# Kernel optimization log

Hardware: AMD Instinct MI355X
Metric: run time of the kernel (lower is better)

## Reference

```python
import jax, jax.numpy as jnp
import numpy as np

N = 10000   # num_nodes
E = 640000  # num_edges (avg degree 64)
IN = 128    # in_feature
HID = 16    # hidden (fixed in __init__)
H = 8       # out_head
ED = 8      # edge_dim
OUT = 3     # out_feature
SLOPE = 0.2 # LeakyReLU alpha in NGATConv

def setup_inputs():
    key = jax.random.key(0)
    k = jax.random.split(key, 16)
    def rn(i, shape, scale=1.0):
        return jax.random.normal(k[i], shape, dtype=jnp.float32) * jnp.float32(scale)
    return {
        "x": rn(0, (N, IN)),
        "edge_attr": rn(1, (E, ED)),
        "fc_w": rn(2, (HID, IN), 1.0 / np.sqrt(IN)),
        "fc_b": jnp.zeros((HID,), jnp.float32),
        "lin_w": rn(3, (H * HID, HID), 1.0 / np.sqrt(HID)),
        "att_src": rn(4, (H, HID), 0.1),
        "att_dst": rn(5, (H, HID), 0.1),
        "att_edge": rn(6, (H, HID), 0.1),
        "lin_edge_w": rn(7, (H * HID, ED), 1.0 / np.sqrt(ED)),
        "conv_bias": jnp.zeros((HID,), jnp.float32),
        "attn_fc_w": rn(8, (1, HID), 1.0 / np.sqrt(HID)),
        "attn_fc_b": jnp.zeros((1,), jnp.float32),
        "out_w": rn(9, (OUT, N * HID), 1.0 / np.sqrt(N * HID)),
        "out_b": jnp.zeros((OUT,), jnp.float32),
        "edge_index": jax.random.randint(k[10], (2, E), 0, N),
    }

def reference(x, edge_attr, fc_w, fc_b, lin_w, att_src, att_dst, att_edge,
              lin_edge_w, conv_bias, attn_fc_w, attn_fc_b, out_w, out_b, edge_index):
    src, dst = edge_index[0], edge_index[1]
    # embed (matrix_in=False path); dropout is identity in eval mode
    h = x @ fc_w.T + fc_b                                   # [N, HID]
    # NGATConv: per-head linear transform
    xp = (h @ lin_w.T).reshape(N, H, HID)                   # [N, H, C]
    a_src = jnp.einsum('nhc,hc->nh', xp, att_src)           # [N, H]
    a_dst = jnp.einsum('nhc,hc->nh', xp, att_dst)           # [N, H]
    ee = (edge_attr @ lin_edge_w.T).reshape(E, H, HID)      # [E, H, C]
    a_edge = jnp.einsum('ehc,hc->eh', ee, att_edge)         # [E, H]
    logits = a_src[src] + a_dst[dst] + a_edge               # [E, H]
    logits = jnp.where(logits >= 0, logits, SLOPE * logits) # LeakyReLU(0.2)
    # segment softmax over incoming edges of each destination node
    m = jax.ops.segment_max(logits, dst, num_segments=N)    # [N, H]
    ex = jnp.exp(logits - m[dst])
    denom = jax.ops.segment_sum(ex, dst, num_segments=N)    # [N, H]
    alpha = ex / (denom[dst] + 1e-16)                       # [E, H]
    # message passing: gather source features, weight, scatter-add to dst
    msg = alpha[:, :, None] * xp[src]                       # [E, H, C]
    agg = jax.ops.segment_sum(msg, dst, num_segments=N)     # [N, H, C]
    out = agg.mean(axis=1) + conv_bias                      # concat=False -> head mean
    out = jax.nn.elu(out)                                   # [N, HID]
    # attention pooling over nodes
    score = out @ attn_fc_w.T + attn_fc_b                   # [N, 1]
    w = jax.nn.softmax(score, axis=0)[:, 0]                 # softmax over node dim
    flat = (out * w[:, None]).reshape(1, -1)                # [1, N*HID]
    y = (flat @ out_w.T + out_b)[0]                         # [OUT]
    # attention weight element [head 0, dst 6, src 6]
    attn_66 = jnp.sum(jnp.where((src == 6) & (dst == 6), alpha[:, 0], jnp.float32(0.0)))
    return y, attn_66
```

## Files before the change

kernel.cpp:

```cpp
#include <hip/hip_runtime.h>
#include <hip/hip_fp16.h>

#define IN_F 128
#define HIDC 16
#define NHEAD 8
#define HHID 128
#define EDIM 8
#define MAXN 10240
#define HB   64
#define FB   128

__global__ __launch_bounds__(256) void k_node_hist(const float* __restrict__ x,
                                                   const float* __restrict__ fc_w,
                                                   const float* __restrict__ fc_b,
                                                   const float* __restrict__ lin_w,
                                                   const float* __restrict__ att_src,
                                                   const float* __restrict__ att_dst,
                                                   const int* __restrict__ ei,
                                                   __half* __restrict__ xp_h,
                                                   float* __restrict__ a_src,
                                                   float* __restrict__ a_dst,
                                                   unsigned short* __restrict__ ph,
                                                   unsigned short* __restrict__ lrank,
                                                   int N, int E, int CHUNK) {
    __shared__ __align__(16) char smem[MAXN * 4];
    int t = threadIdx.x;

    if ((int)blockIdx.x < HB) {
        int* lh = (int*)smem;
        int b = blockIdx.x;
        for (int i = t; i < MAXN; i += 256) lh[i] = 0;
        __syncthreads();
        int e0 = b * CHUNK;
        int e1 = min(e0 + CHUNK, E);
        for (int e = e0 + t; e < e1; e += 256)
            lrank[e] = (unsigned short)atomicAdd(&lh[ei[E + e]], 1);
        __syncthreads();
        for (int nn = t; nn < N; nn += 256)
            ph[(size_t)b * N + nn] = (unsigned short)lh[nn];
        return;
    }

    float* s_x   = (float*)smem;
    float* s_fc  = s_x + 32 * 129;
    float* s_lin = s_fc + 16 * 129;
    float* s_h   = s_lin + 128 * 17;
    float* s_as  = s_h + 32 * 17;
    float* s_ad  = s_as + HHID;
    float* s_fcb = s_ad + HHID;

    int n0 = (blockIdx.x - HB) * 32;

    for (int i = t; i < HIDC * IN_F; i += 256) s_fc[(i >> 7) * 129 + (i & 127)] = fc_w[i];
    for (int i = t; i < HHID * HIDC; i += 256) s_lin[(i >> 4) * 17 + (i & 15)] = lin_w[i];
    if (t < HHID) { s_as[t] = att_src[t]; s_ad[t] = att_dst[t]; }
    if (t < HIDC) s_fcb[t] = fc_b[t];
    for (int i = t; i < 32 * IN_F; i += 256) {
        size_t g = (size_t)n0 * IN_F + i;
        s_x[(i >> 7) * 129 + (i & 127)] = (g < (size_t)N * IN_F) ? x[g] : 0.f;
    }
    __syncthreads();

    {
        int k = t >> 5, n_l = t & 31;
        float a0 = 0.f, a1 = 0.f;
        #pragma unroll 8
        for (int d = 0; d < IN_F; ++d) {
            float xv = s_x[n_l * 129 + d];
            a0 += xv * s_fc[k * 129 + d];
            a1 += xv * s_fc[(k + 8) * 129 + d];
        }
        s_h[n_l * 17 + k]     = a0 + s_fcb[k];
        s_h[n_l * 17 + k + 8] = a1 + s_fcb[k + 8];
    }
    __syncthreads();

    int head = t >> 5, n_l = t & 31;
    int n = n0 + n_l;
    if (n >= N) return;

    float hreg[HIDC];
    #pragma unroll
    for (int k = 0; k < HIDC; ++k) hreg[k] = s_h[n_l * 17 + k];

    float as = 0.f, ad = 0.f;
    unsigned int pk[8];
    #pragma unroll
    for (int c2 = 0; c2 < 8; ++c2) {
        float v2[2];
        #pragma unroll
        for (int u = 0; u < 2; ++u) {
            int c = c2 * 2 + u;
            int j = head * HIDC + c;
            float v = 0.f;
            #pragma unroll
            for (int k = 0; k < HIDC; ++k) v += hreg[k] * s_lin[j * 17 + k];
            v2[u] = v;
            as += v * s_as[j];
            ad += v * s_ad[j];
        }
        unsigned short lo = __half_as_ushort(__float2half_rn(v2[0]));
        unsigned short hi = __half_as_ushort(__float2half_rn(v2[1]));
        pk[c2] = (unsigned int)lo | ((unsigned int)hi << 16);
    }
    __half* xph = xp_h + (size_t)n * HHID + head * HIDC;
    *(uint4*)(xph)     = make_uint4(pk[0], pk[1], pk[2], pk[3]);
    *(uint4*)(xph + 8) = make_uint4(pk[4], pk[5], pk[6], pk[7]);
    a_src[n * NHEAD + head] = as;
    a_dst[n * NHEAD + head] = ad;
}

__global__ __launch_bounds__(256) void k_coloff0(unsigned short* __restrict__ ph,
                                                 int* __restrict__ deg, int N) {
    int n = blockIdx.x * 256 + threadIdx.x;
    if (n >= N) return;
    unsigned short v[HB];
    #pragma unroll
    for (int b = 0; b < HB; ++b) v[b] = ph[(size_t)b * N + n];
    int run = 0;
    #pragma unroll
    for (int b = 0; b < HB; ++b) {
        int c = v[b];
        ph[(size_t)b * N + n] = (unsigned short)run;
        run += c;
    }
    deg[n] = run;
}

__global__ __launch_bounds__(1024) void k_scan(const int* __restrict__ deg,
                                               int* __restrict__ start, int N) {
    const int CH = 16;
    __shared__ int s_w[16];
    int t = threadIdx.x;
    int lane = t & 63, wid = t >> 6;
    int vals[CH];
    int base_i = t * CH;
    int s = 0;
    #pragma unroll
    for (int i = 0; i < CH; ++i) {
        int idx = base_i + i;
        int v = (idx < N) ? deg[idx] : 0;
        vals[i] = v;
        s += v;
    }
    int inc = s;
    #pragma unroll
    for (int off = 1; off < 64; off <<= 1) {
        int u = __shfl_up(inc, off, 64);
        if (lane >= off) inc += u;
    }
    if (lane == 63) s_w[wid] = inc;
    __syncthreads();
    if (wid == 0) {
        int wv = (lane < 16) ? s_w[lane] : 0;
        #pragma unroll
        for (int off = 1; off < 16; off <<= 1) {
            int u = __shfl_up(wv, off, 64);
            if (lane >= off) wv += u;
        }
        if (lane < 16) s_w[lane] = wv;
    }
    __syncthreads();
    int base = inc - s + (wid > 0 ? s_w[wid - 1] : 0);
    #pragma unroll
    for (int i = 0; i < CH; ++i) {
        int idx = base_i + i;
        if (idx < N) start[idx] = base;
        base += vals[i];
    }
    if (t == 0) start[N] = s_w[15];
}

__global__ __launch_bounds__(256) void k_fill(const float* __restrict__ ea,
                                              const int* __restrict__ ei,
                                              const float* __restrict__ a_src,
                                              const float* __restrict__ a_dst,
                                              const float* __restrict__ att_edge,
                                              const float* __restrict__ lin_edge_w,
                                              const int* __restrict__ start,
                                              const unsigned short* __restrict__ ph,
                                              const unsigned short* __restrict__ lrank,
                                              uint4* __restrict__ rec,
                                              int N, int E, int CHUNK) {
    __shared__ float s_w[64];
    int t = threadIdx.x;
    if (t < 64) {
        int h = t >> 3, d = t & 7;
        float s = 0.f;
        #pragma unroll
        for (int c = 0; c < HIDC; ++c)
            s += att_edge[h * HIDC + c] * lin_edge_w[(h * HIDC + c) * EDIM + d];
        s_w[t] = s;
    }
    __syncthreads();
    int e = blockIdx.x * 256 + t;
    if (e >= E) return;

    int s = ei[e];
    int d = ei[E + e];
    int pos = start[d] + (int)ph[(size_t)(e / CHUNK) * N + d] + (int)lrank[e];

    float4 ea0 = *(const float4*)(ea + (size_t)e * EDIM);
    float4 ea1 = *(const float4*)(ea + (size_t)e * EDIM + 4);
    float eav[8] = {ea0.x, ea0.y, ea0.z, ea0.w, ea1.x, ea1.y, ea1.z, ea1.w};

    float4 as0 = *(const float4*)(a_src + (size_t)s * NHEAD);
    float4 as1 = *(const float4*)(a_src + (size_t)s * NHEAD + 4);
    float4 ad0 = *(const float4*)(a_dst + (size_t)d * NHEAD);
    float4 ad1 = *(const float4*)(a_dst + (size_t)d * NHEAD + 4);
    float asv[8] = {as0.x, as0.y, as0.z, as0.w, as1.x, as1.y, as1.z, as1.w};
    float adv[8] = {ad0.x, ad0.y, ad0.z, ad0.w, ad1.x, ad1.y, ad1.z, ad1.w};

    float exs[8];
    #pragma unroll
    for (int h = 0; h < NHEAD; ++h) {
        float aev = 0.f;
        #pragma unroll
        for (int dd = 0; dd < EDIM; ++dd) aev += eav[dd] * s_w[h * EDIM + dd];
        float lg = asv[h] + adv[h] + aev;
        lg = (lg >= 0.f) ? lg : 0.2f * lg;
        exs[h] = __expf(lg);
    }
    unsigned int pk[4];
    #pragma unroll
    for (int j = 0; j < 4; ++j) {
        unsigned short lo = __half_as_ushort(__float2half_rn(exs[2 * j]));
        unsigned short hi = __half_as_ushort(__float2half_rn(exs[2 * j + 1]));
        pk[j] = (unsigned int)lo | ((unsigned int)hi << 16);
    }
    rec[(size_t)pos * 2] = make_uint4(pk[0], pk[1], pk[2], pk[3]);
    ((int*)rec)[(size_t)pos * 8 + 4] = s;
}

__global__ __launch_bounds__(128) void k_gather(const uint4* __restrict__ rec,
                                                const int* __restrict__ start,
                                                const __half* __restrict__ xp_h,
                                                const float* __restrict__ conv_bias,
                                                const float* __restrict__ attn_w,
                                                const float* __restrict__ attn_b,
                                                float* __restrict__ out_feat,
                                                float* __restrict__ score,
                                                float* __restrict__ attn66,
                                                int N) {
    int n = blockIdx.x;
    int t = threadIdx.x;
    int es = t >> 4;
    int v  = t & 15;
    int hv = v >> 1;

    __shared__ int s_s[128];
    __shared__ float s_ex[128 * NHEAD];
    __shared__ float sacc[8 * 128];
    __shared__ float sdenp[128];
    __shared__ float sden[NHEAD];
    __shared__ float sred[128];

    int s0 = start[n];
    int s1 = start[n + 1];

    float acc8[8];
    #pragma unroll
    for (int k = 0; k < 8; ++k) acc8[k] = 0.f;
    float denp = 0.f;
    float a66 = 0.f;

    for (int base = s0; base < s1; base += 128) {
        int m = s1 - base; if (m > 128) m = 128;
        __syncthreads();
        if (t < m) {
            size_t p = (size_t)(base + t);
            uint4 u = rec[p * 2];
            s_s[t] = ((const int*)rec)[p * 8 + 4];
            float2 f0 = __half22float2(*reinterpret_cast<const __half2*>(&u.x));
            float2 f1 = __half22float2(*reinterpret_cast<const __half2*>(&u.y));
            float2 f2 = __half22float2(*reinterpret_cast<const __half2*>(&u.z));
            float2 f3 = __half22float2(*reinterpret_cast<const __half2*>(&u.w));
            float* row = s_ex + t * NHEAD;
            row[0] = f0.x; row[1] = f0.y; row[2] = f1.x; row[3] = f1.y;
            row[4] = f2.x; row[5] = f2.y; row[6] = f3.x; row[7] = f3.y;
        }
        __syncthreads();
        #pragma unroll 2
        for (int i = 0; i < m; i += 8) {
            int e_i = i + es;
            if (e_i < m) {
                const uint4 u = *(const uint4*)(xp_h + (size_t)s_s[e_i] * HHID + v * 8);
                float ev = s_ex[e_i * NHEAD + hv];
                float2 f0 = __half22float2(*reinterpret_cast<const __half2*>(&u.x));
                float2 f1 = __half22float2(*reinterpret_cast<const __half2*>(&u.y));
                float2 f2 = __half22float2(*reinterpret_cast<const __half2*>(&u.z));
                float2 f3 = __half22float2(*reinterpret_cast<const __half2*>(&u.w));
                acc8[0] += ev * f0.x; acc8[1] += ev * f0.y;
                acc8[2] += ev * f1.x; acc8[3] += ev * f1.y;
                acc8[4] += ev * f2.x; acc8[5] += ev * f2.y;
                acc8[6] += ev * f3.x; acc8[7] += ev * f3.y;
            }
        }
        {
            int hh = t >> 4, sl = t & 15;
            for (int i = sl; i < m; i += 16) denp += s_ex[i * NHEAD + hh];
        }
        if (n == 6 && t == 0) {
            for (int i = 0; i < m; ++i)
                if (s_s[i] == 6) a66 += s_ex[i * NHEAD];
        }
    }

    sdenp[t] = denp;
    #pragma unroll
    for (int k = 0; k < 8; ++k) sacc[es * 128 + v * 8 + k] = acc8[k];
    __syncthreads();
    if (t < NHEAD) {
        float dsum = 0.f;
        #pragma unroll
        for (int sl = 0; sl < 16; ++sl) dsum += sdenp[t * 16 + sl];
        sden[t] = dsum;
    }
    __syncthreads();

    float accv = 0.f;
    #pragma unroll
    for (int g = 0; g < 8; ++g) accv += sacc[g * 128 + t];
    accv *= 1.f / (sden[t >> 4] + 1e-16f);
    if (n == 6 && t == 0) attn66[0] = a66 / (sden[0] + 1e-16f);

    sred[t] = accv;
    __syncthreads();
    if (t < HIDC) {
        float sum = 0.f;
        #pragma unroll
        for (int hh = 0; hh < NHEAD; ++hh) sum += sred[hh * HIDC + t];
        float vv = sum * 0.125f + conv_bias[t];
        vv = (vv > 0.f) ? vv : expm1f(vv);
        out_feat[n * HIDC + t] = vv;
        sred[t] = vv * attn_w[t];
    }
    __syncthreads();
    if (t == 0) {
        float sc = 0.f;
        #pragma unroll
        for (int c = 0; c < HIDC; ++c) sc += sred[c];
        score[n] = sc + attn_b[0];
    }
}

__global__ __launch_bounds__(256) void k_final_part(const float* __restrict__ out_feat,
                                                    const float* __restrict__ score,
                                                    const float* __restrict__ out_w,
                                                    float4* __restrict__ part,
                                                    int N) {
    int total = N * HIDC;
    float p0 = 0.f, p1 = 0.f, p2 = 0.f, ps = 0.f;
    for (int i = blockIdx.x * 256 + threadIdx.x; i < total; i += gridDim.x * 256) {
        int n = i >> 4;
        float w = __expf(score[n]);
        float f = out_feat[i] * w;
        p0 += f * out_w[i];
        p1 += f * out_w[total + i];
        p2 += f * out_w[2 * total + i];
        if ((i & 15) == 0) ps += w;
    }
    #pragma unroll
    for (int off = 32; off > 0; off >>= 1) {
        p0 += __shfl_down(p0, off);
        p1 += __shfl_down(p1, off);
        p2 += __shfl_down(p2, off);
        ps += __shfl_down(ps, off);
    }
    __shared__ float sm[4][4];
    int wid = threadIdx.x >> 6;
    if ((threadIdx.x & 63) == 0) {
        sm[wid][0] = p0; sm[wid][1] = p1; sm[wid][2] = p2; sm[wid][3] = ps;
    }
    __syncthreads();
    if (threadIdx.x == 0) {
        float a = 0.f, b = 0.f, c = 0.f, d = 0.f;
        #pragma unroll
        for (int w2 = 0; w2 < 4; ++w2) {
            a += sm[w2][0]; b += sm[w2][1]; c += sm[w2][2]; d += sm[w2][3];
        }
        part[blockIdx.x] = make_float4(a, b, c, d);
    }
}

__global__ __launch_bounds__(128) void k_final_sum(const float4* __restrict__ part,
                                                   const float* __restrict__ out_b,
                                                   const float* __restrict__ attn66,
                                                   float* __restrict__ d_out) {
    int t = threadIdx.x;
    float4 v = (t < FB) ? part[t] : make_float4(0.f, 0.f, 0.f, 0.f);
    float a = v.x, b = v.y, c = v.z, d = v.w;
    #pragma unroll
    for (int off = 32; off > 0; off >>= 1) {
        a += __shfl_down(a, off);
        b += __shfl_down(b, off);
        c += __shfl_down(c, off);
        d += __shfl_down(d, off);
    }
    __shared__ float4 sm[2];
    if ((t & 63) == 0) sm[t >> 6] = make_float4(a, b, c, d);
    __syncthreads();
    if (t == 0) {
        a = sm[0].x + sm[1].x;
        b = sm[0].y + sm[1].y;
        c = sm[0].z + sm[1].z;
        d = sm[0].w + sm[1].w;
        float inv = 1.f / d;
        d_out[0] = a * inv + out_b[0];
        d_out[1] = b * inv + out_b[1];
        d_out[2] = c * inv + out_b[2];
        d_out[3] = attn66[0];
    }
}

extern "C" void kernel_launch(void* const* d_in, const int* in_sizes, int n_in,
                              void* d_out, int out_size, void* d_ws, size_t ws_size,
                              hipStream_t stream) {
    const float* x          = (const float*)d_in[0];
    const float* edge_attr  = (const float*)d_in[1];
    const float* fc_w       = (const float*)d_in[2];
    const float* fc_b       = (const float*)d_in[3];
    const float* lin_w      = (const float*)d_in[4];
    const float* att_src    = (const float*)d_in[5];
    const float* att_dst    = (const float*)d_in[6];
    const float* att_edge   = (const float*)d_in[7];
    const float* lin_edge_w = (const float*)d_in[8];
    const float* conv_bias  = (const float*)d_in[9];
    const float* attn_fc_w  = (const float*)d_in[10];
    const float* attn_fc_b  = (const float*)d_in[11];
    const float* out_w      = (const float*)d_in[12];
    const float* out_b      = (const float*)d_in[13];
    const int*   edge_index = (const int*)d_in[14];
    float* out = (float*)d_out;

    const int N = in_sizes[0] / IN_F;
    const int E = in_sizes[14] / 2;
    const int CHUNK = (E + HB - 1) / HB;

    char* w = (char*)d_ws;
    uint4* rec      = (uint4*)w;           w += (size_t)E * 32;
    float4* part    = (float4*)w;          w += (size_t)FB * 16;
    __half* xp_h    = (__half*)w;          w += (size_t)N * HHID * 2;
    float* a_src    = (float*)w;           w += (size_t)N * NHEAD * 4;
    float* a_dst    = (float*)w;           w += (size_t)N * NHEAD * 4;
    float* out_feat = (float*)w;           w += (size_t)N * HIDC * 4;
    float* score    = (float*)w;           w += (size_t)N * 4;
    float* attn66   = (float*)w;           w += 4;
    int* deg        = (int*)w;             w += (size_t)N * 4;
    int* start      = (int*)w;             w += (size_t)(N + 1) * 4;
    unsigned short* ph    = (unsigned short*)w; w += (size_t)HB * N * 2;
    unsigned short* lrank = (unsigned short*)w; w += (size_t)E * 2;

    const int NB_NODE = (N + 31) / 32;
    k_node_hist<<<HB + NB_NODE, 256, 0, stream>>>(
        x, fc_w, fc_b, lin_w, att_src, att_dst, edge_index,
        xp_h, a_src, a_dst, ph, lrank, N, E, CHUNK);
    k_coloff0<<<(N + 255) / 256, 256, 0, stream>>>(ph, deg, N);
    k_scan<<<1, 1024, 0, stream>>>(deg, start, N);
    k_fill<<<(E + 255) / 256, 256, 0, stream>>>(edge_attr, edge_index, a_src, a_dst,
                                                att_edge, lin_edge_w, start, ph, lrank,
                                                rec, N, E, CHUNK);
    k_gather<<<N, 128, 0, stream>>>(rec, start, xp_h, conv_bias,
                                    attn_fc_w, attn_fc_b, out_feat, score, attn66, N);
    k_final_part<<<FB, 256, 0, stream>>>(out_feat, score, out_w, part, N);
    k_final_sum<<<1, 128, 0, stream>>>(part, out_b, attn66, out);
}
```

Before: 81.15 us.

## Replace per-edge rank array with chunked shared-memory atomic fill; fuse final reduction

The counting sort no longer stores a per-edge local rank. Instead, the fill kernel runs one block per histogram chunk (HB raised to 256) and assigns CSR slots with shared-memory atomics seeded from start plus the chunk offset. This removes the lrank write and read traffic and adds more parallel histogram blocks. The two final reduction kernels are merged into one using a last-block-done counter, which saves a launch. The fill step now runs only 256 blocks and has a serial per-block loop, and the order of edges within a node becomes nondeterministic.

```diff
diff --git a/kernel.cpp b/kernel.cpp
--- a/kernel.cpp
+++ b/kernel.cpp
@@ -7,7 +7,7 @@
 #define HHID 128
 #define EDIM 8
 #define MAXN 10240
-#define HB   64
+#define HB   256
 #define FB   128
 
 __global__ __launch_bounds__(256) void k_node_hist(const float* __restrict__ x,
@@ -21,7 +21,6 @@
                                                    float* __restrict__ a_src,
                                                    float* __restrict__ a_dst,
                                                    unsigned short* __restrict__ ph,
-                                                   unsigned short* __restrict__ lrank,
                                                    int N, int E, int CHUNK) {
     __shared__ __align__(16) char smem[MAXN * 4];
     int t = threadIdx.x;
@@ -34,7 +33,7 @@
         int e0 = b * CHUNK;
         int e1 = min(e0 + CHUNK, E);
         for (int e = e0 + t; e < e1; e += 256)
-            lrank[e] = (unsigned short)atomicAdd(&lh[ei[E + e]], 1);
+            atomicAdd(&lh[ei[E + e]], 1);
         __syncthreads();
         for (int nn = t; nn < N; nn += 256)
             ph[(size_t)b * N + nn] = (unsigned short)lh[nn];
@@ -114,24 +113,29 @@
                                                  int* __restrict__ deg, int N) {
     int n = blockIdx.x * 256 + threadIdx.x;
     if (n >= N) return;
-    unsigned short v[HB];
-    #pragma unroll
-    for (int b = 0; b < HB; ++b) v[b] = ph[(size_t)b * N + n];
     int run = 0;
-    #pragma unroll
-    for (int b = 0; b < HB; ++b) {
-        int c = v[b];
-        ph[(size_t)b * N + n] = (unsigned short)run;
-        run += c;
+    for (int g = 0; g < 4; ++g) {
+        unsigned short v[64];
+        #pragma unroll
+        for (int b = 0; b < 64; ++b)
+            v[b] = ph[(size_t)(g * 64 + b) * N + n];
+        #pragma unroll
+        for (int b = 0; b < 64; ++b) {
+            int c = v[b];
+            ph[(size_t)(g * 64 + b) * N + n] = (unsigned short)run;
+            run += c;
+        }
     }
     deg[n] = run;
 }
 
 __global__ __launch_bounds__(1024) void k_scan(const int* __restrict__ deg,
-                                               int* __restrict__ start, int N) {
+                                               int* __restrict__ start,
+                                               int* __restrict__ fcnt, int N) {
     const int CH = 16;
     __shared__ int s_w[16];
     int t = threadIdx.x;
+    if (t == 0) *fcnt = 0;
     int lane = t & 63, wid = t >> 6;
     int vals[CH];
     int base_i = t * CH;
@@ -179,11 +183,12 @@
                                               const float* __restrict__ lin_edge_w,
                                               const int* __restrict__ start,
                                               const unsigned short* __restrict__ ph,
-                                              const unsigned short* __restrict__ lrank,
                                               uint4* __restrict__ rec,
                                               int N, int E, int CHUNK) {
+    __shared__ int lh[MAXN];
     __shared__ float s_w[64];
     int t = threadIdx.x;
+    int b = blockIdx.x;
     if (t < 64) {
         int h = t >> 3, d = t & 7;
         float s = 0.f;
@@ -192,44 +197,48 @@
             s += att_edge[h * HIDC + c] * lin_edge_w[(h * HIDC + c) * EDIM + d];
         s_w[t] = s;
     }
-    __syncthreads();
-    int e = blockIdx.x * 256 + t;
-    if (e >= E) return;
-
-    int s = ei[e];
-    int d = ei[E + e];
-    int pos = start[d] + (int)ph[(size_t)(e / CHUNK) * N + d] + (int)lrank[e];
-
-    float4 ea0 = *(const float4*)(ea + (size_t)e * EDIM);
-    float4 ea1 = *(const float4*)(ea + (size_t)e * EDIM + 4);
-    float eav[8] = {ea0.x, ea0.y, ea0.z, ea0.w, ea1.x, ea1.y, ea1.z, ea1.w};
-
-    float4 as0 = *(const float4*)(a_src + (size_t)s * NHEAD);
-    float4 as1 = *(const float4*)(a_src + (size_t)s * NHEAD + 4);
-    float4 ad0 = *(const float4*)(a_dst + (size_t)d * NHEAD);
-    float4 ad1 = *(const float4*)(a_dst + (size_t)d * NHEAD + 4);
-    float asv[8] = {as0.x, as0.y, as0.z, as0.w, as1.x, as1.y, as1.z, as1.w};
-    float adv[8] = {ad0.x, ad0.y, ad0.z, ad0.w, ad1.x, ad1.y, ad1.z, ad1.w};
-
-    float exs[8];
-    #pragma unroll
-    for (int h = 0; h < NHEAD; ++h) {
-        float aev = 0.f;
-        #pragma unroll
-        for (int dd = 0; dd < EDIM; ++dd) aev += eav[dd] * s_w[h * EDIM + dd];
-        float lg = asv[h] + adv[h] + aev;
-        lg = (lg >= 0.f) ? lg : 0.2f * lg;
-        exs[h] = __expf(lg);
-    }
-    unsigned int pk[4];
-    #pragma unroll
-    for (int j = 0; j < 4; ++j) {
-        unsigned short lo = __half_as_ushort(__float2half_rn(exs[2 * j]));
-        unsigned short hi = __half_as_ushort(__float2half_rn(exs[2 * j + 1]));
-        pk[j] = (unsigned int)lo | ((unsigned int)hi << 16);
-    }
-    rec[(size_t)pos * 2] = make_uint4(pk[0], pk[1], pk[2], pk[3]);
-    ((int*)rec)[(size_t)pos * 8 + 4] = s;
+    for (int nn = t; nn < N; nn += 256)
+        lh[nn] = start[nn] + (int)ph[(size_t)b * N + nn];
+    __syncthreads();
+
+    int e0 = b * CHUNK;
+    int e1 = min(e0 + CHUNK, E);
+    for (int e = e0 + t; e < e1; e += 256) {
+        int s = ei[e];
+        int d = ei[E + e];
+        int pos = atomicAdd(&lh[d], 1);
+
+        float4 ea0 = *(const float4*)(ea + (size_t)e * EDIM);
+        float4 ea1 = *(const float4*)(ea + (size_t)e * EDIM + 4);
+        float eav[8] = {ea0.x, ea0.y, ea0.z, ea0.w, ea1.x, ea1.y, ea1.z, ea1.w};
+
+        float4 as0 = *(const float4*)(a_src + (size_t)s * NHEAD);
+        float4 as1 = *(const float4*)(a_src + (size_t)s * NHEAD + 4);
+        float4 ad0 = *(const float4*)(a_dst + (size_t)d * NHEAD);
+        float4 ad1 = *(const float4*)(a_dst + (size_t)d * NHEAD + 4);
+        float asv[8] = {as0.x, as0.y, as0.z, as0.w, as1.x, as1.y, as1.z, as1.w};
+        float adv[8] = {ad0.x, ad0.y, ad0.z, ad0.w, ad1.x, ad1.y, ad1.z, ad1.w};
+
+        float exs[8];
+        #pragma unroll
+        for (int h = 0; h < NHEAD; ++h) {
+            float aev = 0.f;
+            #pragma unroll
+            for (int dd = 0; dd < EDIM; ++dd) aev += eav[dd] * s_w[h * EDIM + dd];
+            float lg = asv[h] + adv[h] + aev;
+            lg = (lg >= 0.f) ? lg : 0.2f * lg;
+            exs[h] = __expf(lg);
+        }
+        unsigned int pk[4];
+        #pragma unroll
+        for (int j = 0; j < 4; ++j) {
+            unsigned short lo = __half_as_ushort(__float2half_rn(exs[2 * j]));
+            unsigned short hi = __half_as_ushort(__float2half_rn(exs[2 * j + 1]));
+            pk[j] = (unsigned int)lo | ((unsigned int)hi << 16);
+        }
+        rec[(size_t)pos * 2] = make_uint4(pk[0], pk[1], pk[2], pk[3]);
+        ((int*)rec)[(size_t)pos * 8 + 4] = s;
+    }
 }
 
 __global__ __launch_bounds__(128) void k_gather(const uint4* __restrict__ rec,
@@ -344,11 +353,15 @@
     }
 }
 
-__global__ __launch_bounds__(256) void k_final_part(const float* __restrict__ out_feat,
-                                                    const float* __restrict__ score,
-                                                    const float* __restrict__ out_w,
-                                                    float4* __restrict__ part,
-                                                    int N) {
+__global__ __launch_bounds__(256) void k_final(const float* __restrict__ out_feat,
+                                               const float* __restrict__ score,
+                                               const float* __restrict__ out_w,
+                                               const float* __restrict__ out_b,
+                                               const float* __restrict__ attn66,
+                                               float4* __restrict__ part,
+                                               int* __restrict__ fcnt,
+                                               float* __restrict__ d_out,
+                                               int N) {
     int total = N * HIDC;
     float p0 = 0.f, p1 = 0.f, p2 = 0.f, ps = 0.f;
     for (int i = blockIdx.x * 256 + threadIdx.x; i < total; i += gridDim.x * 256) {
@@ -368,6 +381,7 @@
         ps += __shfl_down(ps, off);
     }
     __shared__ float sm[4][4];
+    __shared__ int s_last;
     int wid = threadIdx.x >> 6;
     if ((threadIdx.x & 63) == 0) {
         sm[wid][0] = p0; sm[wid][1] = p1; sm[wid][2] = p2; sm[wid][3] = ps;
@@ -380,13 +394,13 @@
             a += sm[w2][0]; b += sm[w2][1]; c += sm[w2][2]; d += sm[w2][3];
         }
         part[blockIdx.x] = make_float4(a, b, c, d);
-    }
-}
-
-__global__ __launch_bounds__(128) void k_final_sum(const float4* __restrict__ part,
-                                                   const float* __restrict__ out_b,
-                                                   const float* __restrict__ attn66,
-                                                   float* __restrict__ d_out) {
+        __threadfence();
+        s_last = (atomicAdd(fcnt, 1) == FB - 1);
+    }
+    __syncthreads();
+    if (!s_last) return;
+
+    __threadfence();
     int t = threadIdx.x;
     float4 v = (t < FB) ? part[t] : make_float4(0.f, 0.f, 0.f, 0.f);
     float a = v.x, b = v.y, c = v.z, d = v.w;
@@ -397,14 +411,14 @@
         c += __shfl_down(c, off);
         d += __shfl_down(d, off);
     }
-    __shared__ float4 sm[2];
-    if ((t & 63) == 0) sm[t >> 6] = make_float4(a, b, c, d);
+    __shared__ float4 sm2[4];
+    if ((t & 63) == 0) sm2[t >> 6] = make_float4(a, b, c, d);
     __syncthreads();
     if (t == 0) {
-        a = sm[0].x + sm[1].x;
-        b = sm[0].y + sm[1].y;
-        c = sm[0].z + sm[1].z;
-        d = sm[0].w + sm[1].w;
+        a = sm2[0].x + sm2[1].x;
+        b = sm2[0].y + sm2[1].y;
+        c = sm2[0].z + sm2[1].z;
+        d = sm2[0].w + sm2[1].w;
         float inv = 1.f / d;
         d_out[0] = a * inv + out_b[0];
         d_out[1] = b * inv + out_b[1];
@@ -448,20 +462,19 @@
     float* attn66   = (float*)w;           w += 4;
     int* deg        = (int*)w;             w += (size_t)N * 4;
     int* start      = (int*)w;             w += (size_t)(N + 1) * 4;
-    unsigned short* ph    = (unsigned short*)w; w += (size_t)HB * N * 2;
-    unsigned short* lrank = (unsigned short*)w; w += (size_t)E * 2;
+    int* fcnt       = (int*)w;             w += 4;
+    unsigned short* ph = (unsigned short*)w; w += (size_t)HB * N * 2;
 
     const int NB_NODE = (N + 31) / 32;
     k_node_hist<<<HB + NB_NODE, 256, 0, stream>>>(
         x, fc_w, fc_b, lin_w, att_src, att_dst, edge_index,
-        xp_h, a_src, a_dst, ph, lrank, N, E, CHUNK);
+        xp_h, a_src, a_dst, ph, N, E, CHUNK);
     k_coloff0<<<(N + 255) / 256, 256, 0, stream>>>(ph, deg, N);
-    k_scan<<<1, 1024, 0, stream>>>(deg, start, N);
-    k_fill<<<(E + 255) / 256, 256, 0, stream>>>(edge_attr, edge_index, a_src, a_dst,
-                                                att_edge, lin_edge_w, start, ph, lrank,
-                                                rec, N, E, CHUNK);
+    k_scan<<<1, 1024, 0, stream>>>(deg, start, fcnt, N);
+    k_fill<<<HB, 256, 0, stream>>>(edge_attr, edge_index, a_src, a_dst,
+                                   att_edge, lin_edge_w, start, ph, rec, N, E, CHUNK);
     k_gather<<<N, 128, 0, stream>>>(rec, start, xp_h, conv_bias,
                                     attn_fc_w, attn_fc_b, out_feat, score, attn66, N);
-    k_final_part<<<FB, 256, 0, stream>>>(out_feat, score, out_w, part, N);
-    k_final_sum<<<1, 128, 0, stream>>>(part, out_b, attn66, out);
-}
+    k_final<<<FB, 256, 0, stream>>>(out_feat, score, out_w, out_b, attn66,
+                                    part, fcnt, out, N);
+}
```

New measurement: 88.06 us. 8.5% more time.
